# Kernel optimization log

Hardware: AMD Instinct MI355X
Metric: run time of the kernel (lower is better)

The kernel has to match this reference:

```python
import jax, jax.numpy as jnp
import numpy as np

B, T = 256, 1024
V, E, H = 27, 64, 128


def setup_inputs() -> dict:
    key = jax.random.key(0)
    ks = jax.random.split(key, 8)
    return {
        "x": jax.random.randint(ks[0], (B, T), 0, V, dtype=jnp.int32),
        "emb": jax.random.normal(ks[1], (V, E), dtype=jnp.float32) * 0.02,
        "wx0": jax.random.normal(ks[2], (E, 4 * H), dtype=jnp.float32) * 0.01,
        "wh0": jax.random.normal(ks[3], (H, 4 * H), dtype=jnp.float32) * 0.01,
        "b0": jnp.zeros((4 * H,), dtype=jnp.float32),
        "wx1": jax.random.normal(ks[4], (H, 4 * H), dtype=jnp.float32) * 0.01,
        "wh1": jax.random.normal(ks[5], (H, 4 * H), dtype=jnp.float32) * 0.01,
        "b1": jnp.zeros((4 * H,), dtype=jnp.float32),
        "why": jax.random.normal(ks[6], (H, V), dtype=jnp.float32),
        "by": jnp.zeros((V,), dtype=jnp.float32),
    }


def _cell(xt, h_prev, c_prev, wx, wh, b):
    # gates: [B, 4H]; chunk order matches torch .chunk(4): f, i, g, o
    gates = xt @ wx + h_prev @ wh + b
    ft, it, gt, ot = jnp.split(gates, 4, axis=1)
    c_t = jax.nn.sigmoid(ft) * c_prev + jax.nn.sigmoid(it) * jnp.tanh(gt)
    h_t = jnp.tanh(c_t) * jax.nn.sigmoid(ot)
    return h_t, c_t


def reference(x, emb, wx0, wh0, b0, wx1, wh1, b1, why, by):
    Bx = x.shape[0]
    xe = emb[x]                       # [B, T, E]
    xe = jnp.swapaxes(xe, 0, 1)       # [T, B, E] for scan over time
    h0 = jnp.zeros((Bx, H), jnp.float32)
    c0 = jnp.zeros((Bx, H), jnp.float32)
    h1 = jnp.zeros((Bx, H), jnp.float32)
    c1 = jnp.zeros((Bx, H), jnp.float32)

    def step(carry, xt):
        h0, c0, h1, c1 = carry
        h0, c0 = _cell(xt, h0, c0, wx0, wh0, b0)   # layer 0
        h1, c1 = _cell(h0, h1, c1, wx1, wh1, b1)   # layer 1 (dropout off in eval)
        yt = h1 @ why + by                         # [B, V]
        return (h0, c0, h1, c1), yt

    _, ys = jax.lax.scan(step, (h0, c0, h1, c1), xe)  # ys: [T, B, V]
    return jnp.swapaxes(ys, 0, 1)                     # [B, T, V]
```

## Files before the change

kernel.cpp:

```cpp
#include <hip/hip_runtime.h>


#define B_  256
#define T_  1024
#define V_  27
#define E_  64
#define H_  128
#define G4  512
#define TPITCH 528

typedef float v2f __attribute__((ext_vector_type(2)));

__device__ __forceinline__ v2f mkv2(float a, float b) { v2f r; r.x = a; r.y = b; return r; }

template <int CTRL>
__device__ __forceinline__ float dppmov(float v) {
    return __int_as_float(__builtin_amdgcn_update_dpp(
               0, __float_as_int(v), CTRL, 0xF, 0xF, true));
}
__device__ __forceinline__ float qsum(float v) {
    v += dppmov<0xB1>(v);
    v += dppmov<0x4E>(v);
    return v;
}
__device__ __forceinline__ float tanh_fast(float y) {
    const float t = __expf(2.f * y);
    return fmaf(-2.f, __builtin_amdgcn_rcpf(t + 1.f), 1.f);
}

#define REPEAT16(M) M(0) M(1) M(2) M(3) M(4) M(5) M(6) M(7) \
                    M(8) M(9) M(10) M(11) M(12) M(13) M(14) M(15)

#define DECLW(K) v2f wf##K, wi##K, wg##K, wo##K;
#define LOADW(K) { const float* r0 = wmat + (size_t)(kb + 2*(K)) * G4; \
                   wf##K = mkv2(r0[p],          r0[G4 + p]); \
                   wi##K = mkv2(r0[H_ + p],     r0[G4 + H_ + p]); \
                   wg##K = mkv2(r0[2*H_ + p],   r0[G4 + 2*H_ + p]); \
                   wo##K = mkv2(r0[3*H_ + p],   r0[G4 + 3*H_ + p]); }
#define PINW(K) asm("" : "+v"(wf##K), "+v"(wi##K), "+v"(wg##K), "+v"(wo##K));
#define FMAP(K, HA, HB) { const v2f h2 = mkv2(HA, HB); \
    sf2 = __builtin_elementwise_fma(h2, wf##K, sf2); \
    si2 = __builtin_elementwise_fma(h2, wi##K, si2); \
    sg2 = __builtin_elementwise_fma(h2, wg##K, sg2); \
    so2 = __builtin_elementwise_fma(h2, wo##K, so2); }

#define FMABODY \
    v2f sf2 = mkv2(0.f, 0.f), si2 = sf2, sg2 = sf2, so2 = sf2; \
    FMAP(0,  v0.x, v0.y) FMAP(1,  v0.z, v0.w) \
    FMAP(2,  v1.x, v1.y) FMAP(3,  v1.z, v1.w) \
    FMAP(4,  v2.x, v2.y) FMAP(5,  v2.z, v2.w) \
    FMAP(6,  v3.x, v3.y) FMAP(7,  v3.z, v3.w) \
    FMAP(8,  v4.x, v4.y) FMAP(9,  v4.z, v4.w) \
    FMAP(10, v5.x, v5.y) FMAP(11, v5.z, v5.w) \
    FMAP(12, v6.x, v6.y) FMAP(13, v6.z, v6.w) \
    FMAP(14, v7.x, v7.y) FMAP(15, v7.z, v7.w)

__global__ __launch_bounds__(G4)
void build_table0(const float* __restrict__ emb,
                  const float* __restrict__ wx0,
                  const float* __restrict__ b0,
                  float* __restrict__ table0)
{
    const int v = blockIdx.x;
    const int j = threadIdx.x;
    __shared__ float e[E_];
    if (j < E_) e[j] = emb[v * E_ + j];
    __syncthreads();
    float s = b0[j];
#pragma unroll 8
    for (int k = 0; k < E_; ++k) s = fmaf(e[k], wx0[k * G4 + j], s);
    const int r = j & (H_ - 1), gate = j >> 7;
    table0[v * TPITCH + gate * 132 + r] = s;
}

__global__ __launch_bounds__(512, 2)
void lstm_l0_chunk(const int* __restrict__ x,
                   const float* __restrict__ table0,
                   const float* __restrict__ wh0,
                   float* __restrict__ h0st, float* __restrict__ c0st,
                   float* __restrict__ h0buf,
                   int t0, int TC)
{
    const int j = threadIdx.x;
    const int p = j >> 2;
    const int e = j & 3;
    const int b = blockIdx.x;
    const int kb = 32 * e;

    __shared__ __align__(16) float hP[2][4][36];

    const float* wmat = wh0;
    REPEAT16(DECLW)
    REPEAT16(LOADW)
    if (j < H_) hP[0][j >> 5][j & 31] = h0st[b * H_ + j];
    float c = c0st[b * H_ + p];
    float hh = 0.f;
    __syncthreads();

    const int* xb = x + (size_t)b * T_ + t0;
    float* hob = h0buf + (size_t)b * TC * H_;
    const float A = (e == 2) ? 2.f : 1.f;
    const int toff = (e & 3) * 132 + p;

    float tv = table0[xb[0] * TPITCH + toff];
    for (int t = 0; t < TC; ++t) {
        REPEAT16(PINW)
        const int idxn = (t + 1 < TC) ? xb[t + 1] : 0;

        const float4* hb4 = reinterpret_cast<const float4*>(&hP[t & 1][e][0]);
        const float4 v0 = hb4[0], v1 = hb4[1], v2 = hb4[2], v3 = hb4[3],
                     v4 = hb4[4], v5 = hb4[5], v6 = hb4[6], v7 = hb4[7];
        FMABODY
        const float sf = qsum(sf2.x + sf2.y);
        const float si = qsum(si2.x + si2.y);
        const float sg = qsum(sg2.x + sg2.y);
        const float so = qsum(so2.x + so2.y);

        float val = (e == 0) ? sf : (e == 1) ? si : (e == 2) ? sg : so;
        val += tv;
        const float tz  = __expf(A * val);
        const float act = fmaf(-A, __builtin_amdgcn_rcpf(tz + 1.f), 1.f);

        const float iv = dppmov<0x39>(act);
        const float gv = dppmov<0x4E>(act);
        const float ov = dppmov<0x93>(act);
        c  = fmaf(act, c, iv * gv);
        hh = tanh_fast(c) * ov;

        if (e == 0) {
            hP[(t + 1) & 1][p >> 5][p & 31] = hh;
            hob[(size_t)t * H_ + p] = hh;
        }
        tv = table0[idxn * TPITCH + toff];
        __syncthreads();
    }
    if (e == 0) { h0st[b * H_ + p] = hh; c0st[b * H_ + p] = c; }
}

__global__ __launch_bounds__(G4, 2)
void gemm_xg1(const float* __restrict__ h0buf,
              const float* __restrict__ wx1,
              const float* __restrict__ b1,
              float* __restrict__ xg1)
{
    const int j  = threadIdx.x;
    const size_t m0 = (size_t)blockIdx.x * 64;
    const int c  = j & 127;
    const int rg = j >> 7;

    __shared__ __align__(16) float aT[64 * 132];

#pragma unroll
    for (int i = 0; i < 4; ++i) {
        const int e  = i * G4 + j;
        const int r  = e >> 5;
        const int k4 = e & 31;
        const float4 v = *reinterpret_cast<const float4*>(&h0buf[(m0 + r) * H_ + k4 * 4]);
        *reinterpret_cast<float4*>(&aT[r * 132 + k4 * 4]) = v;
    }
    __syncthreads();

    float acc[4][16];
#pragma unroll
    for (int cc = 0; cc < 4; ++cc)
#pragma unroll
        for (int rr = 0; rr < 16; ++rr) acc[cc][rr] = 0.f;

    for (int k4 = 0; k4 < 32; ++k4) {
        float bv[4][4];
#pragma unroll
        for (int kk = 0; kk < 4; ++kk)
#pragma unroll
            for (int cc = 0; cc < 4; ++cc)
                bv[kk][cc] = wx1[(size_t)(k4 * 4 + kk) * G4 + cc * 128 + c];
#pragma unroll
        for (int rr = 0; rr < 16; ++rr) {
            const float4 av = *reinterpret_cast<const float4*>(&aT[(rg * 16 + rr) * 132 + k4 * 4]);
#pragma unroll
            for (int cc = 0; cc < 4; ++cc) {
                acc[cc][rr] = fmaf(av.x, bv[0][cc], acc[cc][rr]);
                acc[cc][rr] = fmaf(av.y, bv[1][cc], acc[cc][rr]);
                acc[cc][rr] = fmaf(av.z, bv[2][cc], acc[cc][rr]);
                acc[cc][rr] = fmaf(av.w, bv[3][cc], acc[cc][rr]);
            }
        }
    }

    float b1v[4];
#pragma unroll
    for (int cc = 0; cc < 4; ++cc) b1v[cc] = b1[cc * 128 + c];
#pragma unroll
    for (int rr = 0; rr < 16; ++rr) {
        const size_t row = m0 + rg * 16 + rr;
#pragma unroll
        for (int cc = 0; cc < 4; ++cc)
            xg1[row * G4 + cc * 128 + c] = acc[cc][rr] + b1v[cc];
    }
}

__global__ __launch_bounds__(512, 2)
void lstm_l1_chunk(const float* __restrict__ xg1,
                   const float* __restrict__ wh1,
                   float* __restrict__ h1st, float* __restrict__ c1st,
                   float* __restrict__ h1buf,
                   int TC)
{
    const int j = threadIdx.x;
    const int p = j >> 2;
    const int e = j & 3;
    const int b = blockIdx.x;
    const int kb = 32 * e;

    __shared__ __align__(16) float hP[2][4][36];

    const float* wmat = wh1;
    REPEAT16(DECLW)
    REPEAT16(LOADW)
    if (j < H_) hP[0][j >> 5][j & 31] = h1st[b * H_ + j];
    float c = c1st[b * H_ + p];
    float hh = 0.f;
    __syncthreads();

    const float* xgb = xg1 + (size_t)b * TC * G4;
    float* hob = h1buf + (size_t)b * TC * H_;
    const float A = (e == 2) ? 2.f : 1.f;
    const int xcol = e * H_ + p;

    float xv = xgb[xcol];
    for (int t = 0; t < TC; ++t) {
        REPEAT16(PINW)
        const float xvn = (t + 1 < TC) ? xgb[(size_t)(t + 1) * G4 + xcol] : 0.f;

        const float4* hb4 = reinterpret_cast<const float4*>(&hP[t & 1][e][0]);
        const float4 v0 = hb4[0], v1 = hb4[1], v2 = hb4[2], v3 = hb4[3],
                     v4 = hb4[4], v5 = hb4[5], v6 = hb4[6], v7 = hb4[7];
        FMABODY
        const float sf = qsum(sf2.x + sf2.y);
        const float si = qsum(si2.x + si2.y);
        const float sg = qsum(sg2.x + sg2.y);
        const float so = qsum(so2.x + so2.y);

        float val = (e == 0) ? sf : (e == 1) ? si : (e == 2) ? sg : so;
        val += xv;
        const float tz  = __expf(A * val);
        const float act = fmaf(-A, __builtin_amdgcn_rcpf(tz + 1.f), 1.f);

        const float iv = dppmov<0x39>(act);
        const float gv = dppmov<0x4E>(act);
        const float ov = dppmov<0x93>(act);
        c  = fmaf(act, c, iv * gv);
        hh = tanh_fast(c) * ov;

        if (e == 0) {
            hP[(t + 1) & 1][p >> 5][p & 31] = hh;
            hob[(size_t)t * H_ + p] = hh;
        }
        xv = xvn;
        __syncthreads();
    }
    if (e == 0) { h1st[b * H_ + p] = hh; c1st[b * H_ + p] = c; }
}

__global__ __launch_bounds__(256)
void proj_y(const float* __restrict__ h1buf,
            const float* __restrict__ why,
            const float* __restrict__ by,
            float* __restrict__ out,
            int t0, int TC)
{
    const int tid = threadIdx.x;
    const int b   = blockIdx.x;

    __shared__ __align__(16) float whyS[V_][H_];
    __shared__ float byS[V_];
    __shared__ float yS[256][29];

    for (int e = tid; e < V_ * H_; e += 256) {
        const int v = e / H_, k = e - v * H_;
        whyS[v][k] = why[k * V_ + v];
    }
    if (tid < V_) byS[tid] = by[tid];
    __syncthreads();

    const float* hb  = h1buf + (size_t)b * TC * H_;
    float* outb      = out + ((size_t)b * T_ + t0) * V_;

    for (int tt0 = 0; tt0 < TC; tt0 += 256) {
        const int tt = tt0 + tid;
        if (tt < TC) {
            float acc[V_];
#pragma unroll
            for (int v = 0; v < V_; ++v) acc[v] = byS[v];
            const float4* hr = reinterpret_cast<const float4*>(hb + (size_t)tt * H_);
#pragma unroll 4
            for (int k4 = 0; k4 < 32; ++k4) {
                const float4 hv = hr[k4];
#pragma unroll
                for (int v = 0; v < V_; ++v) {
                    const float4 wv = *reinterpret_cast<const float4*>(&whyS[v][k4 * 4]);
                    acc[v] = fmaf(hv.x, wv.x,
                             fmaf(hv.y, wv.y,
                             fmaf(hv.z, wv.z,
                             fmaf(hv.w, wv.w, acc[v]))));
                }
            }
#pragma unroll
            for (int v = 0; v < V_; ++v) yS[tid][v] = acc[v];
        }
        __syncthreads();
        const int nrow = (TC - tt0 < 256) ? (TC - tt0) : 256;
        const int n = nrow * V_;
        float* od = outb + (size_t)tt0 * V_;
        for (int i = tid; i < n; i += 256) {
            const int r = i / V_, v = i - r * V_;
            od[i] = yS[r][v];
        }
        __syncthreads();
    }
}

__global__ __launch_bounds__(G4, 1)
void lstm_persist(const int* __restrict__ x,
                  const float* __restrict__ table0,
                  const float* __restrict__ wh0,
                  const float* __restrict__ wx1,
                  const float* __restrict__ wh1,
                  const float* __restrict__ b1,
                  const float* __restrict__ why,
                  const float* __restrict__ by,
                  float* __restrict__ out)
{
    const int j  = threadIdx.x;
    const int bb = blockIdx.x * 2;

    __shared__ float h0s[2][H_], c0s[2][H_], h1s[2][H_], c1s[2][H_];
    __shared__ float hcat[2][2 * H_];
    __shared__ float g0s[2][G4], g1s[2][G4];
    __shared__ float whyS[H_ * V_];
    __shared__ float b1S[G4];
    __shared__ float byS[V_];
    __shared__ float pb[2][V_][8];

    for (int i = j; i < H_ * V_; i += G4) whyS[i] = why[i];
    b1S[j] = b1[j];
    if (j < V_) byS[j] = by[j];
    if (j < H_) {
        h0s[0][j] = 0.f; h0s[1][j] = 0.f; c0s[0][j] = 0.f; c0s[1][j] = 0.f;
        h1s[0][j] = 0.f; h1s[1][j] = 0.f; c1s[0][j] = 0.f; c1s[1][j] = 0.f;
    }
    __syncthreads();

    const int* xA = x + (size_t)(bb + 0) * T_;
    const int* xB = x + (size_t)(bb + 1) * T_;
    float* outA = out + (size_t)(bb + 0) * T_ * V_;
    float* outB = out + (size_t)(bb + 1) * T_ * V_;

    const int tix = (j >> 7) * 132 + (j & (H_ - 1));

    for (int t = 0; t < T_; ++t) {
        const int ia = xA[t];
        const int ib = xB[t];
        float aA = table0[ia * TPITCH + tix];
        float aB = table0[ib * TPITCH + tix];
#pragma unroll 8
        for (int k = 0; k < H_; ++k) {
            const float w = wh0[k * G4 + j];
            aA += h0s[0][k] * w;
            aB += h0s[1][k] * w;
        }
        g0s[0][j] = aA; g0s[1][j] = aB;
        __syncthreads();

        if (j < 2 * H_) {
            const int gi = j >> 7, r = j & (H_ - 1);
            const float f  = 1.f / (1.f + expf(-g0s[gi][r]));
            const float i_ = 1.f / (1.f + expf(-g0s[gi][H_ + r]));
            const float g  = tanhf(g0s[gi][2 * H_ + r]);
            const float o  = 1.f / (1.f + expf(-g0s[gi][3 * H_ + r]));
            const float c  = f * c0s[gi][r] + i_ * g;
            c0s[gi][r] = c;
            const float h = tanhf(c) * o;
            h0s[gi][r] = h;
            hcat[gi][r] = h;
            hcat[gi][H_ + r] = h1s[gi][r];
        }
        __syncthreads();

        float bA = b1S[j];
        float bB = bA;
#pragma unroll 8
        for (int k = 0; k < H_; ++k) {
            const float w = wx1[k * G4 + j];
            bA += hcat[0][k] * w;
            bB += hcat[1][k] * w;
        }
#pragma unroll 8
        for (int k = 0; k < H_; ++k) {
            const float w = wh1[k * G4 + j];
            bA += hcat[0][H_ + k] * w;
            bB += hcat[1][H_ + k] * w;
        }
        g1s[0][j] = bA; g1s[1][j] = bB;
        __syncthreads();

        if (j < 2 * H_) {
            const int gi = j >> 7, r = j & (H_ - 1);
            const float f  = 1.f / (1.f + expf(-g1s[gi][r]));
            const float i_ = 1.f / (1.f + expf(-g1s[gi][H_ + r]));
            const float g  = tanhf(g1s[gi][2 * H_ + r]);
            const float o  = 1.f / (1.f + expf(-g1s[gi][3 * H_ + r]));
            const float c  = f * c1s[gi][r] + i_ * g;
            c1s[gi][r] = c;
            h1s[gi][r] = tanhf(c) * o;
        }
        __syncthreads();

        if (j < 2 * V_ * 8) {
            int qq = j;
            const int gi = (qq >= V_ * 8) ? 1 : 0;
            qq -= gi * V_ * 8;
            const int v = qq >> 3, kk = qq & 7;
            float pv = 0.f;
#pragma unroll
            for (int k = kk * 16; k < kk * 16 + 16; ++k)
                pv += h1s[gi][k] * whyS[k * V_ + v];
            pb[gi][v][kk] = pv;
        }
        __syncthreads();

        if (j < 2 * V_) {
            const int gi = (j >= V_) ? 1 : 0;
            const int v  = j - gi * V_;
            float sA = byS[v];
#pragma unroll
            for (int qq = 0; qq < 8; ++qq) sA += pb[gi][v][qq];
            (gi ? outB : outA)[t * V_ + v] = sA;
        }
        __syncthreads();
    }
}

extern "C" void kernel_launch(void* const* d_in, const int* in_sizes, int n_in,
                              void* d_out, int out_size, void* d_ws, size_t ws_size,
                              hipStream_t stream)
{
    const int*   x   = (const int*)  d_in[0];
    const float* emb = (const float*)d_in[1];
    const float* wx0 = (const float*)d_in[2];
    const float* wh0 = (const float*)d_in[3];
    const float* b0  = (const float*)d_in[4];
    const float* wx1 = (const float*)d_in[5];
    const float* wh1 = (const float*)d_in[6];
    const float* b1  = (const float*)d_in[7];
    const float* why = (const float*)d_in[8];
    const float* by  = (const float*)d_in[9];
    float* out = (float*)d_out;
    float* wsf = (float*)d_ws;

    const size_t tabF   = (size_t)V_ * TPITCH;
    const size_t stateF = (size_t)4 * B_ * H_;

    int TC = 0;
    for (int tc = T_; tc >= 32; tc >>= 1) {
        const size_t need = (tabF + stateF + (size_t)B_ * tc * (H_ + G4 + H_)) * 4;
        if (need <= ws_size) { TC = tc; break; }
    }

    float* table0 = wsf;
    build_table0<<<dim3(V_), dim3(G4), 0, stream>>>(emb, wx0, b0, table0);

    if (TC == 0) {
        lstm_persist<<<dim3(B_ / 2), dim3(G4), 0, stream>>>(
            x, table0, wh0, wx1, wh1, b1, why, by, out);
        return;
    }

    float* h0st   = wsf + tabF;
    float* c0st   = h0st + (size_t)B_ * H_;
    float* h1st   = c0st + (size_t)B_ * H_;
    float* c1st   = h1st + (size_t)B_ * H_;
    float* h0buf  = c1st + (size_t)B_ * H_;
    float* xg1buf = h0buf + (size_t)B_ * TC * H_;
    float* h1buf  = xg1buf + (size_t)B_ * TC * G4;

    (void)hipMemsetAsync(h0st, 0, stateF * sizeof(float), stream);

    const int NC = T_ / TC;
    for (int c = 0; c < NC; ++c) {
        const int t0 = c * TC;
        lstm_l0_chunk<<<dim3(B_), dim3(512), 0, stream>>>(
            x, table0, wh0, h0st, c0st, h0buf, t0, TC);
        gemm_xg1<<<dim3(4 * TC), dim3(G4), 0, stream>>>(
            h0buf, wx1, b1, xg1buf);
        lstm_l1_chunk<<<dim3(B_), dim3(512), 0, stream>>>(
            xg1buf, wh1, h1st, c1st, h1buf, TC);
        proj_y<<<dim3(B_), dim3(256), 0, stream>>>(
            h1buf, why, by, out, t0, TC);
    }
}
```

Before: 1.871 ms.

## Pipeline LSTM layers across chunks with two-batch-row blocks

Each recurrent block now processes two batch rows, interleaving their independent FMA chains and reductions to raise instruction-level parallelism in the latency-bound step loop. A fused kernel runs layer 1 on chunk c in half the blocks while the other half runs layer 0 on chunk c+1, so both recurrences advance in the same launch instead of serially. Prologue and epilogue kernels handle the first layer-0 chunk and the last layer-1 chunk, and the maximum chunk length is capped at 256. The cost is more registers and per-step work per block, plus extra launches from the smaller chunks.

```diff
diff --git a/kernel.cpp b/kernel.cpp
--- a/kernel.cpp
+++ b/kernel.cpp
@@ -38,22 +38,21 @@
                    wg##K = mkv2(r0[2*H_ + p],   r0[G4 + 2*H_ + p]); \
                    wo##K = mkv2(r0[3*H_ + p],   r0[G4 + 3*H_ + p]); }
 #define PINW(K) asm("" : "+v"(wf##K), "+v"(wi##K), "+v"(wg##K), "+v"(wo##K));
-#define FMAP(K, HA, HB) { const v2f h2 = mkv2(HA, HB); \
-    sf2 = __builtin_elementwise_fma(h2, wf##K, sf2); \
-    si2 = __builtin_elementwise_fma(h2, wi##K, si2); \
-    sg2 = __builtin_elementwise_fma(h2, wg##K, sg2); \
-    so2 = __builtin_elementwise_fma(h2, wo##K, so2); }
-
-#define FMABODY \
-    v2f sf2 = mkv2(0.f, 0.f), si2 = sf2, sg2 = sf2, so2 = sf2; \
-    FMAP(0,  v0.x, v0.y) FMAP(1,  v0.z, v0.w) \
-    FMAP(2,  v1.x, v1.y) FMAP(3,  v1.z, v1.w) \
-    FMAP(4,  v2.x, v2.y) FMAP(5,  v2.z, v2.w) \
-    FMAP(6,  v3.x, v3.y) FMAP(7,  v3.z, v3.w) \
-    FMAP(8,  v4.x, v4.y) FMAP(9,  v4.z, v4.w) \
-    FMAP(10, v5.x, v5.y) FMAP(11, v5.z, v5.w) \
-    FMAP(12, v6.x, v6.y) FMAP(13, v6.z, v6.w) \
-    FMAP(14, v7.x, v7.y) FMAP(15, v7.z, v7.w)
+#define FMAP2(K, HA, HB, SF, SI, SG, SO) { const v2f h2 = mkv2(HA, HB); \
+    SF = __builtin_elementwise_fma(h2, wf##K, SF); \
+    SI = __builtin_elementwise_fma(h2, wi##K, SI); \
+    SG = __builtin_elementwise_fma(h2, wg##K, SG); \
+    SO = __builtin_elementwise_fma(h2, wo##K, SO); }
+
+#define FMABODY2(U, SF, SI, SG, SO) \
+    FMAP2(0,  (U##0).x, (U##0).y, SF, SI, SG, SO) FMAP2(1,  (U##0).z, (U##0).w, SF, SI, SG, SO) \
+    FMAP2(2,  (U##1).x, (U##1).y, SF, SI, SG, SO) FMAP2(3,  (U##1).z, (U##1).w, SF, SI, SG, SO) \
+    FMAP2(4,  (U##2).x, (U##2).y, SF, SI, SG, SO) FMAP2(5,  (U##2).z, (U##2).w, SF, SI, SG, SO) \
+    FMAP2(6,  (U##3).x, (U##3).y, SF, SI, SG, SO) FMAP2(7,  (U##3).z, (U##3).w, SF, SI, SG, SO) \
+    FMAP2(8,  (U##4).x, (U##4).y, SF, SI, SG, SO) FMAP2(9,  (U##4).z, (U##4).w, SF, SI, SG, SO) \
+    FMAP2(10, (U##5).x, (U##5).y, SF, SI, SG, SO) FMAP2(11, (U##5).z, (U##5).w, SF, SI, SG, SO) \
+    FMAP2(12, (U##6).x, (U##6).y, SF, SI, SG, SO) FMAP2(13, (U##6).z, (U##6).w, SF, SI, SG, SO) \
+    FMAP2(14, (U##7).x, (U##7).y, SF, SI, SG, SO) FMAP2(15, (U##7).z, (U##7).w, SF, SI, SG, SO)
 
 __global__ __launch_bounds__(G4)
 void build_table0(const float* __restrict__ emb,
@@ -73,68 +72,231 @@
     table0[v * TPITCH + gate * 132 + r] = s;
 }
 
-__global__ __launch_bounds__(512, 2)
-void lstm_l0_chunk(const int* __restrict__ x,
-                   const float* __restrict__ table0,
-                   const float* __restrict__ wh0,
-                   float* __restrict__ h0st, float* __restrict__ c0st,
-                   float* __restrict__ h0buf,
-                   int t0, int TC)
-{
-    const int j = threadIdx.x;
+__device__ __forceinline__ void l0_body2(
+    const int j, const int bb,
+    const int* __restrict__ x, const float* __restrict__ table0,
+    const float* __restrict__ wh0,
+    float* __restrict__ h0st, float* __restrict__ c0st,
+    float* __restrict__ h0buf, int t0, int TC,
+    float (*hPA)[4][36], float (*hPB)[4][36])
+{
     const int p = j >> 2;
     const int e = j & 3;
-    const int b = blockIdx.x;
     const int kb = 32 * e;
-
-    __shared__ __align__(16) float hP[2][4][36];
 
     const float* wmat = wh0;
     REPEAT16(DECLW)
     REPEAT16(LOADW)
-    if (j < H_) hP[0][j >> 5][j & 31] = h0st[b * H_ + j];
-    float c = c0st[b * H_ + p];
-    float hh = 0.f;
+    if (j < H_) {
+        hPA[0][j >> 5][j & 31] = h0st[(size_t)bb * H_ + j];
+        hPB[0][j >> 5][j & 31] = h0st[(size_t)(bb + 1) * H_ + j];
+    }
+    float cA = c0st[(size_t)bb * H_ + p];
+    float cB = c0st[(size_t)(bb + 1) * H_ + p];
+    float hhA = 0.f, hhB = 0.f;
     __syncthreads();
 
-    const int* xb = x + (size_t)b * T_ + t0;
-    float* hob = h0buf + (size_t)b * TC * H_;
+    const int* xbA = x + (size_t)bb * T_ + t0;
+    const int* xbB = x + (size_t)(bb + 1) * T_ + t0;
+    float* hobA = h0buf + (size_t)bb * TC * H_;
+    float* hobB = h0buf + (size_t)(bb + 1) * TC * H_;
     const float A = (e == 2) ? 2.f : 1.f;
-    const int toff = (e & 3) * 132 + p;
-
-    float tv = table0[xb[0] * TPITCH + toff];
+    const int toff = e * 132 + p;
+
+    float tvA = table0[xbA[0] * TPITCH + toff];
+    float tvB = table0[xbB[0] * TPITCH + toff];
     for (int t = 0; t < TC; ++t) {
         REPEAT16(PINW)
-        const int idxn = (t + 1 < TC) ? xb[t + 1] : 0;
-
-        const float4* hb4 = reinterpret_cast<const float4*>(&hP[t & 1][e][0]);
-        const float4 v0 = hb4[0], v1 = hb4[1], v2 = hb4[2], v3 = hb4[3],
-                     v4 = hb4[4], v5 = hb4[5], v6 = hb4[6], v7 = hb4[7];
-        FMABODY
-        const float sf = qsum(sf2.x + sf2.y);
-        const float si = qsum(si2.x + si2.y);
-        const float sg = qsum(sg2.x + sg2.y);
-        const float so = qsum(so2.x + so2.y);
-
-        float val = (e == 0) ? sf : (e == 1) ? si : (e == 2) ? sg : so;
-        val += tv;
-        const float tz  = __expf(A * val);
-        const float act = fmaf(-A, __builtin_amdgcn_rcpf(tz + 1.f), 1.f);
-
-        const float iv = dppmov<0x39>(act);
-        const float gv = dppmov<0x4E>(act);
-        const float ov = dppmov<0x93>(act);
-        c  = fmaf(act, c, iv * gv);
-        hh = tanh_fast(c) * ov;
+        const int idxnA = (t + 1 < TC) ? xbA[t + 1] : 0;
+        const int idxnB = (t + 1 < TC) ? xbB[t + 1] : 0;
+
+        const float4* ha4 = reinterpret_cast<const float4*>(&hPA[t & 1][e][0]);
+        const float4 uA0 = ha4[0], uA1 = ha4[1], uA2 = ha4[2], uA3 = ha4[3],
+                     uA4 = ha4[4], uA5 = ha4[5], uA6 = ha4[6], uA7 = ha4[7];
+        v2f sfA = mkv2(0.f, 0.f), siA = sfA, sgA = sfA, soA = sfA;
+        FMABODY2(uA, sfA, siA, sgA, soA)
+
+        const float4* hb4 = reinterpret_cast<const float4*>(&hPB[t & 1][e][0]);
+        const float4 uB0 = hb4[0], uB1 = hb4[1], uB2 = hb4[2], uB3 = hb4[3],
+                     uB4 = hb4[4], uB5 = hb4[5], uB6 = hb4[6], uB7 = hb4[7];
+        v2f sfB = mkv2(0.f, 0.f), siB = sfB, sgB = sfB, soB = sfB;
+        FMABODY2(uB, sfB, siB, sgB, soB)
+
+        const float rfA = qsum(sfA.x + sfA.y);
+        const float riA = qsum(siA.x + siA.y);
+        const float rgA = qsum(sgA.x + sgA.y);
+        const float roA = qsum(soA.x + soA.y);
+        const float rfB = qsum(sfB.x + sfB.y);
+        const float riB = qsum(siB.x + siB.y);
+        const float rgB = qsum(sgB.x + sgB.y);
+        const float roB = qsum(soB.x + soB.y);
+
+        float valA = (e == 0) ? rfA : (e == 1) ? riA : (e == 2) ? rgA : roA;
+        float valB = (e == 0) ? rfB : (e == 1) ? riB : (e == 2) ? rgB : roB;
+        valA += tvA; valB += tvB;
+        const float actA = fmaf(-A, __builtin_amdgcn_rcpf(__expf(A * valA) + 1.f), 1.f);
+        const float actB = fmaf(-A, __builtin_amdgcn_rcpf(__expf(A * valB) + 1.f), 1.f);
+
+        const float ivA = dppmov<0x39>(actA);
+        const float gvA = dppmov<0x4E>(actA);
+        const float ovA = dppmov<0x93>(actA);
+        cA  = fmaf(actA, cA, ivA * gvA);
+        hhA = tanh_fast(cA) * ovA;
+        const float ivB = dppmov<0x39>(actB);
+        const float gvB = dppmov<0x4E>(actB);
+        const float ovB = dppmov<0x93>(actB);
+        cB  = fmaf(actB, cB, ivB * gvB);
+        hhB = tanh_fast(cB) * ovB;
 
         if (e == 0) {
-            hP[(t + 1) & 1][p >> 5][p & 31] = hh;
-            hob[(size_t)t * H_ + p] = hh;
-        }
-        tv = table0[idxn * TPITCH + toff];
-        __syncthreads();
-    }
-    if (e == 0) { h0st[b * H_ + p] = hh; c0st[b * H_ + p] = c; }
+            hPA[(t + 1) & 1][p >> 5][p & 31] = hhA;
+            hPB[(t + 1) & 1][p >> 5][p & 31] = hhB;
+            hobA[(size_t)t * H_ + p] = hhA;
+            hobB[(size_t)t * H_ + p] = hhB;
+        }
+        tvA = table0[idxnA * TPITCH + toff];
+        tvB = table0[idxnB * TPITCH + toff];
+        __syncthreads();
+    }
+    if (e == 0) {
+        h0st[(size_t)bb * H_ + p] = hhA;       c0st[(size_t)bb * H_ + p] = cA;
+        h0st[(size_t)(bb + 1) * H_ + p] = hhB; c0st[(size_t)(bb + 1) * H_ + p] = cB;
+    }
+}
+
+__device__ __forceinline__ void l1_body2(
+    const int j, const int bb,
+    const float* __restrict__ xg1, const float* __restrict__ wh1,
+    float* __restrict__ h1st, float* __restrict__ c1st,
+    float* __restrict__ h1buf, int TC,
+    float (*hPA)[4][36], float (*hPB)[4][36])
+{
+    const int p = j >> 2;
+    const int e = j & 3;
+    const int kb = 32 * e;
+
+    const float* wmat = wh1;
+    REPEAT16(DECLW)
+    REPEAT16(LOADW)
+    if (j < H_) {
+        hPA[0][j >> 5][j & 31] = h1st[(size_t)bb * H_ + j];
+        hPB[0][j >> 5][j & 31] = h1st[(size_t)(bb + 1) * H_ + j];
+    }
+    float cA = c1st[(size_t)bb * H_ + p];
+    float cB = c1st[(size_t)(bb + 1) * H_ + p];
+    float hhA = 0.f, hhB = 0.f;
+    __syncthreads();
+
+    const float* xgA = xg1 + (size_t)bb * TC * G4;
+    const float* xgB = xg1 + (size_t)(bb + 1) * TC * G4;
+    float* hobA = h1buf + (size_t)bb * TC * H_;
+    float* hobB = h1buf + (size_t)(bb + 1) * TC * H_;
+    const float A = (e == 2) ? 2.f : 1.f;
+    const int xcol = e * H_ + p;
+
+    float xvA = xgA[xcol];
+    float xvB = xgB[xcol];
+    for (int t = 0; t < TC; ++t) {
+        REPEAT16(PINW)
+        const float xvnA = (t + 1 < TC) ? xgA[(size_t)(t + 1) * G4 + xcol] : 0.f;
+        const float xvnB = (t + 1 < TC) ? xgB[(size_t)(t + 1) * G4 + xcol] : 0.f;
+
+        const float4* ha4 = reinterpret_cast<const float4*>(&hPA[t & 1][e][0]);
+        const float4 uA0 = ha4[0], uA1 = ha4[1], uA2 = ha4[2], uA3 = ha4[3],
+                     uA4 = ha4[4], uA5 = ha4[5], uA6 = ha4[6], uA7 = ha4[7];
+        v2f sfA = mkv2(0.f, 0.f), siA = sfA, sgA = sfA, soA = sfA;
+        FMABODY2(uA, sfA, siA, sgA, soA)
+
+        const float4* hb4 = reinterpret_cast<const float4*>(&hPB[t & 1][e][0]);
+        const float4 uB0 = hb4[0], uB1 = hb4[1], uB2 = hb4[2], uB3 = hb4[3],
+                     uB4 = hb4[4], uB5 = hb4[5], uB6 = hb4[6], uB7 = hb4[7];
+        v2f sfB = mkv2(0.f, 0.f), siB = sfB, sgB = sfB, soB = sfB;
+        FMABODY2(uB, sfB, siB, sgB, soB)
+
+        const float rfA = qsum(sfA.x + sfA.y);
+        const float riA = qsum(siA.x + siA.y);
+        const float rgA = qsum(sgA.x + sgA.y);
+        const float roA = qsum(soA.x + soA.y);
+        const float rfB = qsum(sfB.x + sfB.y);
+        const float riB = qsum(siB.x + siB.y);
+        const float rgB = qsum(sgB.x + sgB.y);
+        const float roB = qsum(soB.x + soB.y);
+
+        float valA = (e == 0) ? rfA : (e == 1) ? riA : (e == 2) ? rgA : roA;
+        float valB = (e == 0) ? rfB : (e == 1) ? riB : (e == 2) ? rgB : roB;
+        valA += xvA; valB += xvB;
+        const float actA = fmaf(-A, __builtin_amdgcn_rcpf(__expf(A * valA) + 1.f), 1.f);
+        const float actB = fmaf(-A, __builtin_amdgcn_rcpf(__expf(A * valB) + 1.f), 1.f);
+
+        const float ivA = dppmov<0x39>(actA);
+        const float gvA = dppmov<0x4E>(actA);
+        const float ovA = dppmov<0x93>(actA);
+        cA  = fmaf(actA, cA, ivA * gvA);
+        hhA = tanh_fast(cA) * ovA;
+        const float ivB = dppmov<0x39>(actB);
+        const float gvB = dppmov<0x4E>(actB);
+        const float ovB = dppmov<0x93>(actB);
+        cB  = fmaf(actB, cB, ivB * gvB);
+        hhB = tanh_fast(cB) * ovB;
+
+        if (e == 0) {
+            hPA[(t + 1) & 1][p >> 5][p & 31] = hhA;
+            hPB[(t + 1) & 1][p >> 5][p & 31] = hhB;
+            hobA[(size_t)t * H_ + p] = hhA;
+            hobB[(size_t)t * H_ + p] = hhB;
+        }
+        xvA = xvnA; xvB = xvnB;
+        __syncthreads();
+    }
+    if (e == 0) {
+        h1st[(size_t)bb * H_ + p] = hhA;       c1st[(size_t)bb * H_ + p] = cA;
+        h1st[(size_t)(bb + 1) * H_ + p] = hhB; c1st[(size_t)(bb + 1) * H_ + p] = cB;
+    }
+}
+
+__global__ __launch_bounds__(512, 2)
+void lstm_l0_2b(const int* __restrict__ x, const float* __restrict__ table0,
+                const float* __restrict__ wh0,
+                float* __restrict__ h0st, float* __restrict__ c0st,
+                float* __restrict__ h0buf, int t0, int TC)
+{
+    __shared__ __align__(16) float hPA[2][4][36];
+    __shared__ __align__(16) float hPB[2][4][36];
+    l0_body2(threadIdx.x, 2 * blockIdx.x, x, table0, wh0, h0st, c0st, h0buf,
+             t0, TC, hPA, hPB);
+}
+
+__global__ __launch_bounds__(512, 2)
+void lstm_l1_2b(const float* __restrict__ xg1, const float* __restrict__ wh1,
+                float* __restrict__ h1st, float* __restrict__ c1st,
+                float* __restrict__ h1buf, int TC)
+{
+    __shared__ __align__(16) float hPA[2][4][36];
+    __shared__ __align__(16) float hPB[2][4][36];
+    l1_body2(threadIdx.x, 2 * blockIdx.x, xg1, wh1, h1st, c1st, h1buf, TC,
+             hPA, hPB);
+}
+
+__global__ __launch_bounds__(512, 2)
+void lstm_fused2(const int* __restrict__ x, const float* __restrict__ table0,
+                 const float* __restrict__ wh0,
+                 const float* __restrict__ xg1, const float* __restrict__ wh1,
+                 float* __restrict__ h0st, float* __restrict__ c0st,
+                 float* __restrict__ h0buf,
+                 float* __restrict__ h1st, float* __restrict__ c1st,
+                 float* __restrict__ h1buf,
+                 int t0_l0, int TC)
+{
+    __shared__ __align__(16) float hPA[2][4][36];
+    __shared__ __align__(16) float hPB[2][4][36];
+    const int bid = blockIdx.x;
+    if (bid < B_ / 2) {
+        l1_body2(threadIdx.x, 2 * bid, xg1, wh1, h1st, c1st, h1buf, TC,
+                 hPA, hPB);
+    } else {
+        l0_body2(threadIdx.x, 2 * (bid - B_ / 2), x, table0, wh0,
+                 h0st, c0st, h0buf, t0_l0, TC, hPA, hPB);
+    }
 }
 
 __global__ __launch_bounds__(G4, 2)
@@ -196,69 +358,6 @@
         for (int cc = 0; cc < 4; ++cc)
             xg1[row * G4 + cc * 128 + c] = acc[cc][rr] + b1v[cc];
     }
-}
-
-__global__ __launch_bounds__(512, 2)
-void lstm_l1_chunk(const float* __restrict__ xg1,
-                   const float* __restrict__ wh1,
-                   float* __restrict__ h1st, float* __restrict__ c1st,
-                   float* __restrict__ h1buf,
-                   int TC)
-{
-    const int j = threadIdx.x;
-    const int p = j >> 2;
-    const int e = j & 3;
-    const int b = blockIdx.x;
-    const int kb = 32 * e;
-
-    __shared__ __align__(16) float hP[2][4][36];
-
-    const float* wmat = wh1;
-    REPEAT16(DECLW)
-    REPEAT16(LOADW)
-    if (j < H_) hP[0][j >> 5][j & 31] = h1st[b * H_ + j];
-    float c = c1st[b * H_ + p];
-    float hh = 0.f;
-    __syncthreads();
-
-    const float* xgb = xg1 + (size_t)b * TC * G4;
-    float* hob = h1buf + (size_t)b * TC * H_;
-    const float A = (e == 2) ? 2.f : 1.f;
-    const int xcol = e * H_ + p;
-
-    float xv = xgb[xcol];
-    for (int t = 0; t < TC; ++t) {
-        REPEAT16(PINW)
-        const float xvn = (t + 1 < TC) ? xgb[(size_t)(t + 1) * G4 + xcol] : 0.f;
-
-        const float4* hb4 = reinterpret_cast<const float4*>(&hP[t & 1][e][0]);
-        const float4 v0 = hb4[0], v1 = hb4[1], v2 = hb4[2], v3 = hb4[3],
-                     v4 = hb4[4], v5 = hb4[5], v6 = hb4[6], v7 = hb4[7];
-        FMABODY
-        const float sf = qsum(sf2.x + sf2.y);
-        const float si = qsum(si2.x + si2.y);
-        const float sg = qsum(sg2.x + sg2.y);
-        const float so = qsum(so2.x + so2.y);
-
-        float val = (e == 0) ? sf : (e == 1) ? si : (e == 2) ? sg : so;
-        val += xv;
-        const float tz  = __expf(A * val);
-        const float act = fmaf(-A, __builtin_amdgcn_rcpf(tz + 1.f), 1.f);
-
-        const float iv = dppmov<0x39>(act);
-        const float gv = dppmov<0x4E>(act);
-        const float ov = dppmov<0x93>(act);
-        c  = fmaf(act, c, iv * gv);
-        hh = tanh_fast(c) * ov;
-
-        if (e == 0) {
-            hP[(t + 1) & 1][p >> 5][p & 31] = hh;
-            hob[(size_t)t * H_ + p] = hh;
-        }
-        xv = xvn;
-        __syncthreads();
-    }
-    if (e == 0) { h1st[b * H_ + p] = hh; c1st[b * H_ + p] = c; }
 }
 
 __global__ __launch_bounds__(256)
@@ -461,7 +560,7 @@
     const size_t stateF = (size_t)4 * B_ * H_;
 
     int TC = 0;
-    for (int tc = T_; tc >= 32; tc >>= 1) {
+    for (int tc = 256; tc >= 32; tc >>= 1) {
         const size_t need = (tabF + stateF + (size_t)B_ * tc * (H_ + G4 + H_)) * 4;
         if (need <= ws_size) { TC = tc; break; }
     }
@@ -486,15 +585,23 @@
     (void)hipMemsetAsync(h0st, 0, stateF * sizeof(float), stream);
 
     const int NC = T_ / TC;
-    for (int c = 0; c < NC; ++c) {
-        const int t0 = c * TC;
-        lstm_l0_chunk<<<dim3(B_), dim3(512), 0, stream>>>(
-            x, table0, wh0, h0st, c0st, h0buf, t0, TC);
-        gemm_xg1<<<dim3(4 * TC), dim3(G4), 0, stream>>>(
-            h0buf, wx1, b1, xg1buf);
-        lstm_l1_chunk<<<dim3(B_), dim3(512), 0, stream>>>(
-            xg1buf, wh1, h1st, c1st, h1buf, TC);
+
+    lstm_l0_2b<<<dim3(B_ / 2), dim3(512), 0, stream>>>(
+        x, table0, wh0, h0st, c0st, h0buf, 0, TC);
+    gemm_xg1<<<dim3(4 * TC), dim3(G4), 0, stream>>>(h0buf, wx1, b1, xg1buf);
+
+    for (int c = 0; c < NC - 1; ++c) {
+        lstm_fused2<<<dim3(B_), dim3(512), 0, stream>>>(
+            x, table0, wh0, xg1buf, wh1,
+            h0st, c0st, h0buf, h1st, c1st, h1buf,
+            (c + 1) * TC, TC);
+        gemm_xg1<<<dim3(4 * TC), dim3(G4), 0, stream>>>(h0buf, wx1, b1, xg1buf);
         proj_y<<<dim3(B_), dim3(256), 0, stream>>>(
-            h1buf, why, by, out, t0, TC);
-    }
-}
+            h1buf, why, by, out, c * TC, TC);
+    }
+
+    lstm_l1_2b<<<dim3(B_ / 2), dim3(512), 0, stream>>>(
+        xg1buf, wh1, h1st, c1st, h1buf, TC);
+    proj_y<<<dim3(B_), dim3(256), 0, stream>>>(
+        h1buf, why, by, out, (NC - 1) * TC, TC);
+}
```

New measurement: 2.027 ms. +8.3%, slower.
